# Optimization experiments

Measured on AMD Instinct MI355X. Metric: run time of the kernel, lower is better.

The kernel has to match this reference:

```python
import jax, jax.numpy as jnp
import numpy as np

N, C_IN, C_OUT = 8192, 256, 128
NEG_SLOPE = 0.2


def setup_inputs() -> dict:
    key = jax.random.key(0)
    k0, k1, k2, k3, k4 = jax.random.split(key, 5)
    x = jax.random.normal(k0, (N, C_IN), dtype=jnp.float32)
    # sparse-ish binary dense adjacency, avg degree ~32
    adj = (jax.random.uniform(k1, (N, N)) < (32.0 / N)).astype(jnp.float32)
    W = jax.random.normal(k2, (C_IN, C_OUT), dtype=jnp.float32) * 0.05
    att_src = jax.random.normal(k3, (C_OUT,), dtype=jnp.float32) * 0.1
    att_dst = jax.random.normal(k4, (C_OUT,), dtype=jnp.float32) * 0.1
    bias = jnp.zeros((C_OUT,), dtype=jnp.float32)
    return {"x": x, "adj": adj, "W": W, "att_src": att_src,
            "att_dst": att_dst, "bias": bias}


def reference(x, adj, W, att_src, att_dst, bias):
    n = adj.shape[0]
    idx = jnp.arange(n)
    adj = adj.at[idx, idx].set(1.0)          # add self loops
    h = x @ W                                 # [N, C_out]
    a_src = h @ att_src                       # [N]
    a_dst = h @ att_dst                       # [N]
    alpha = a_src[:, None] + a_dst[None, :]   # [N, N]
    alpha = jax.nn.leaky_relu(alpha, NEG_SLOPE)
    alpha = adj * jnp.exp(alpha)              # masked exp
    alpha = alpha / alpha.sum(axis=0, keepdims=True)  # column-normalize (dim=0)
    out = (adj * alpha).T @ h + bias          # [N, C_out]
    return out
```

## Files before the change

kernel.cpp:

```cpp
#include <hip/hip_runtime.h>
#include <hip/hip_bf16.h>

#define NN 8192
#define CIN 256
#define COUT 128
#define GR 32
#define GKT 64
#define CH 16
#define ICH (NN / CH)
#define KT 64
#define HTS 72

typedef unsigned short u16;
typedef _Float16 f16;
typedef __attribute__((ext_vector_type(8))) short short8;
typedef __attribute__((ext_vector_type(8))) _Float16 f16x8;
typedef __attribute__((ext_vector_type(16))) float f32x16;

__device__ __forceinline__ short8 pack8_bf16(const float* v) {
    union { __hip_bfloat162 b2[4]; short8 s; } u;
    #pragma unroll
    for (int q = 0; q < 4; ++q)
        u.b2[q] = __float22bfloat162_rn(make_float2(v[2 * q], v[2 * q + 1]));
    return u.s;
}

__global__ __launch_bounds__(256) void gemm_h(const float* __restrict__ x,
                                              const float* __restrict__ W,
                                              const float* __restrict__ att_src,
                                              const float* __restrict__ att_dst,
                                              u16* __restrict__ h_t,
                                              float* __restrict__ a_src,
                                              float* __restrict__ a_dst) {
    __shared__ float Wt[GKT * COUT];
    __shared__ float xt[GKT][GR + 4];
    __shared__ float ot[GR][COUT + 4];
    int tid = threadIdx.x;
    int i0 = blockIdx.x * GR;
    int tx = tid & 31, ty = tid >> 5;
    int c0 = tx * 4, r0 = ty * 4;
    int xr = tid >> 3, xk = (tid & 7) * 8;
    float acc[4][4] = {};

    for (int kt = 0; kt < CIN; kt += GKT) {
        float4 wv[8];
        #pragma unroll
        for (int j = 0; j < 8; ++j) {
            int f = j * 256 + tid;
            wv[j] = *(const float4*)&W[(size_t)(kt + (f >> 5)) * COUT + (f & 31) * 4];
        }
        float4 xv0 = *(const float4*)&x[(size_t)(i0 + xr) * CIN + kt + xk];
        float4 xv1 = *(const float4*)&x[(size_t)(i0 + xr) * CIN + kt + xk + 4];
        __syncthreads();
        #pragma unroll
        for (int j = 0; j < 8; ++j)
            *(float4*)&Wt[(j * 256 + tid) * 4] = wv[j];
        xt[xk + 0][xr] = xv0.x; xt[xk + 1][xr] = xv0.y;
        xt[xk + 2][xr] = xv0.z; xt[xk + 3][xr] = xv0.w;
        xt[xk + 4][xr] = xv1.x; xt[xk + 5][xr] = xv1.y;
        xt[xk + 6][xr] = xv1.z; xt[xk + 7][xr] = xv1.w;
        __syncthreads();
        #pragma unroll 8
        for (int k = 0; k < GKT; ++k) {
            float4 wk = *(const float4*)&Wt[k * COUT + c0];
            float4 xf = *(const float4*)&xt[k][r0];
            float xa[4] = {xf.x, xf.y, xf.z, xf.w};
            #pragma unroll
            for (int a = 0; a < 4; ++a) {
                acc[a][0] += xa[a] * wk.x; acc[a][1] += xa[a] * wk.y;
                acc[a][2] += xa[a] * wk.z; acc[a][3] += xa[a] * wk.w;
            }
        }
    }

    float4 asv = *(const float4*)&att_src[c0];
    float4 adv = *(const float4*)&att_dst[c0];
    #pragma unroll
    for (int a = 0; a < 4; ++a) {
        float4 o = make_float4(acc[a][0], acc[a][1], acc[a][2], acc[a][3]);
        *(float4*)&ot[r0 + a][c0] = o;
        float s = o.x * asv.x + o.y * asv.y + o.z * asv.z + o.w * asv.w;
        float d = o.x * adv.x + o.y * adv.y + o.z * adv.z + o.w * adv.w;
        #pragma unroll
        for (int m = 16; m >= 1; m >>= 1) {
            s += __shfl_xor(s, m, 32);
            d += __shfl_xor(d, m, 32);
        }
        if (tx == 0) {
            a_src[i0 + r0 + a] = s;
            a_dst[i0 + r0 + a] = d;
        }
    }
    __syncthreads();
    int c = tid >> 1, hf = tid & 1;
    float vals[16];
    #pragma unroll
    for (int q = 0; q < 16; ++q) vals[q] = ot[hf * 16 + q][c];
    *(short8*)(h_t + (size_t)c * NN + i0 + hf * 16)     = pack8_bf16(vals);
    *(short8*)(h_t + (size_t)c * NN + i0 + hf * 16 + 8) = pack8_bf16(vals + 8);
}

__global__ __launch_bounds__(256, 3) void gat_mm(const float* __restrict__ adj,
                                                 const u16* __restrict__ h_t,
                                                 const float* __restrict__ a_src,
                                                 const float* __restrict__ a_dst,
                                                 f16* __restrict__ pout,
                                                 float* __restrict__ pden) {
    __shared__ unsigned int maskS[KT * 4];
    __shared__ u16 htS[128 * HTS];
    __shared__ float asrcS[ICH];
    int tid = threadIdx.x;
    int lane = tid & 63, w = tid >> 6;
    int jb = blockIdx.x & 63, ch = blockIdx.x >> 6;
    int j0 = jb * 128;
    int i0 = ch * ICH;
    int half = lane >> 5;
    int jloc = w * 32 + (lane & 31);
    int gj = j0 + jloc;
    int slot = lane & 3;
    int kbit = jloc >> 2;
    float dj = a_dst[gj];
    if (tid < ICH / 4)
        ((float4*)asrcS)[tid] = ((const float4*)(a_src + i0))[tid];

    f32x16 acc[4];
    #pragma unroll
    for (int nt = 0; nt < 4; ++nt)
        #pragma unroll
        for (int q = 0; q < 16; ++q) acc[nt][q] = 0.f;
    float dsum = 0.f;
    __syncthreads();

    for (int s = 0; s < ICH / KT; ++s) {
        int ib = i0 + s * KT;
        float4 v[8];
        #pragma unroll
        for (int q = 0; q < 8; ++q) {
            int f = q * 256 + tid;
            v[q] = *(const float4*)&adj[(size_t)(ib + (f >> 5)) * NN + j0 + (f & 31) * 4];
        }
        short8 bv[4]; int bc[4], bi[4];
        #pragma unroll
        for (int q = 0; q < 4; ++q) {
            int p = q * 256 + tid;
            bc[q] = p >> 3; bi[q] = (p & 7) * 8;
            bv[q] = *(const short8*)(h_t + (size_t)bc[q] * NN + ib + bi[q]);
        }
        #pragma unroll
        for (int q = 0; q < 8; ++q) {
            unsigned long long b0 = __ballot(v[q].x != 0.f);
            unsigned long long b1 = __ballot(v[q].y != 0.f);
            unsigned long long b2 = __ballot(v[q].z != 0.f);
            unsigned long long b3 = __ballot(v[q].w != 0.f);
            unsigned long long bb = slot == 0 ? b0 : slot == 1 ? b1
                                  : slot == 2 ? b2 : b3;
            unsigned int mw = (unsigned int)(bb >> (half * 32));
            int R = q * 8 + w * 2 + half;
            if ((lane & 31) < 4) maskS[R * 4 + slot] = mw;
        }
        #pragma unroll
        for (int q = 0; q < 4; ++q)
            *(short8*)(htS + bc[q] * HTS + bi[q]) = bv[q];
        __syncthreads();

        #pragma unroll
        for (int kk = 0; kk < 4; ++kk) {
            int kb = kk * 16 + half * 8;
            int gib = ib + kb;
            short8 bf[4];
            #pragma unroll
            for (int nt = 0; nt < 4; ++nt)
                bf[nt] = *(const short8*)(htS + (nt * 32 + (lane & 31)) * HTS + kb);
            float pv[8];
            #pragma unroll
            for (int e = 0; e < 8; ++e) {
                unsigned int mw = maskS[(kb + e) * 4 + slot];
                float t = asrcS[s * KT + kb + e] + dj;
                float ev = __expf(fmaxf(t, 0.2f * t));
                bool on = ((mw >> kbit) & 1u) | (gib + e == gj);
                pv[e] = on ? ev : 0.f;
                dsum += pv[e];
            }
            short8 af = pack8_bf16(pv);
            #pragma unroll
            for (int nt = 0; nt < 4; ++nt)
                acc[nt] = __builtin_amdgcn_mfma_f32_32x32x16_bf16(af, bf[nt],
                                                                  acc[nt], 0, 0, 0);
        }
        __syncthreads();
    }

    #pragma unroll
    for (int nt = 0; nt < 4; ++nt) {
        int c = nt * 32 + (lane & 31);
        #pragma unroll
        for (int r = 0; r < 16; ++r) {
            int row = (r & 3) + 8 * (r >> 2) + 4 * half;
            int j = j0 + w * 32 + row;
            pout[((size_t)ch * NN + j) * COUT + c] = (f16)acc[nt][r];
        }
    }
    float dall = dsum + __shfl_xor(dsum, 32, 64);
    if (half == 0) pden[(size_t)ch * NN + gj] = dall;
}

__global__ __launch_bounds__(256) void gat_reduce(const f16* __restrict__ pout,
                                                  const float* __restrict__ pden,
                                                  const float* __restrict__ bias,
                                                  float* __restrict__ out) {
    int idx = blockIdx.x * 256 + threadIdx.x;
    int j = idx >> 4;
    int c8 = (idx & 15) * 8;
    float den = 0.f;
    #pragma unroll
    for (int ch = 0; ch < CH; ++ch) den += pden[(size_t)ch * NN + j];
    float s[8] = {};
    #pragma unroll
    for (int ch = 0; ch < CH; ++ch) {
        f16x8 pv = *(const f16x8*)(pout + ((size_t)ch * NN + j) * COUT + c8);
        #pragma unroll
        for (int q = 0; q < 8; ++q) s[q] += (float)pv[q];
    }
    float inv = 1.0f / den;
    float4 b0 = *(const float4*)&bias[c8];
    float4 b1 = *(const float4*)&bias[c8 + 4];
    float4 o0 = make_float4(s[0] * inv + b0.x, s[1] * inv + b0.y,
                            s[2] * inv + b0.z, s[3] * inv + b0.w);
    float4 o1 = make_float4(s[4] * inv + b1.x, s[5] * inv + b1.y,
                            s[6] * inv + b1.z, s[7] * inv + b1.w);
    *(float4*)&out[(size_t)j * COUT + c8]     = o0;
    *(float4*)&out[(size_t)j * COUT + c8 + 4] = o1;
}

extern "C" void kernel_launch(void* const* d_in, const int* in_sizes, int n_in,
                              void* d_out, int out_size, void* d_ws, size_t ws_size,
                              hipStream_t stream) {
    const float* x       = (const float*)d_in[0];
    const float* adj     = (const float*)d_in[1];
    const float* W       = (const float*)d_in[2];
    const float* att_src = (const float*)d_in[3];
    const float* att_dst = (const float*)d_in[4];
    const float* bias    = (const float*)d_in[5];
    float* out = (float*)d_out;

    u16*   h_t   = (u16*)d_ws;
    float* a_src = (float*)((char*)d_ws + (size_t)2 * 1024 * 1024);
    float* a_dst = a_src + NN;
    float* pden  = a_dst + NN;
    f16*   pout  = (f16*)(pden + (size_t)CH * NN);

    gemm_h    <<<NN / GR, 256, 0, stream>>>(x, W, att_src, att_dst, h_t, a_src, a_dst);
    gat_mm    <<<64 * CH, 256, 0, stream>>>(adj, h_t, a_src, a_dst, pout, pden);
    gat_reduce<<<NN * COUT / 8 / 256, 256, 0, stream>>>(pout, pden, bias, out);
}
```

Baseline: 407.0 us.

## Precompute adjacency bitmask in a separate pass and stream it into gat_mm

Adds an adj2mask kernel that reads the dense fp32 adjacency once, ballots nonzero entries into bit words, and writes them in a layout blocked by column tile (maskT). gat_mm then loads one 32-bit mask word per thread per k-step instead of eight float4 adjacency loads plus ballots. The main loop becomes lighter and less memory-bound. The cost is an extra kernel launch and a 8 MB mask write/read round trip; the full 256 MB adjacency is still read once, now with row-contiguous access.

Result: slower. 436.6 us (+7.3%).

```diff
diff --git a/kernel.cpp b/kernel.cpp
--- a/kernel.cpp
+++ b/kernel.cpp
@@ -23,6 +23,35 @@
     for (int q = 0; q < 4; ++q)
         u.b2[q] = __float22bfloat162_rn(make_float2(v[2 * q], v[2 * q + 1]));
     return u.s;
+}
+
+__global__ __launch_bounds__(256) void adj2mask(const float* __restrict__ adj,
+                                                unsigned int* __restrict__ maskT) {
+    int tid = threadIdx.x;
+    int lane = tid & 63, w = tid >> 6;
+    int i = blockIdx.x * 4 + w;
+    const float4* rowp = (const float4*)(adj + (size_t)i * NN);
+    int half = lane >> 5, slot = lane & 3;
+    bool writer = (lane & 31) < 4;
+    for (int it = 0; it < 32; it += 8) {
+        float4 v[8];
+        #pragma unroll
+        for (int q = 0; q < 8; ++q)
+            v[q] = rowp[(it + q) * 64 + lane];
+        #pragma unroll
+        for (int q = 0; q < 8; ++q) {
+            unsigned long long b0 = __ballot(v[q].x != 0.f);
+            unsigned long long b1 = __ballot(v[q].y != 0.f);
+            unsigned long long b2 = __ballot(v[q].z != 0.f);
+            unsigned long long b3 = __ballot(v[q].w != 0.f);
+            unsigned long long bb = slot == 0 ? b0 : slot == 1 ? b1
+                                  : slot == 2 ? b2 : b3;
+            unsigned int mw = (unsigned int)(bb >> (half * 32));
+            int jb = (it + q) * 2 + half;
+            if (writer)
+                maskT[((size_t)jb * NN + i) * 4 + slot] = mw;
+        }
+    }
 }
 
 __global__ __launch_bounds__(256) void gemm_h(const float* __restrict__ x,
@@ -100,7 +129,7 @@
     *(short8*)(h_t + (size_t)c * NN + i0 + hf * 16 + 8) = pack8_bf16(vals + 8);
 }
 
-__global__ __launch_bounds__(256, 3) void gat_mm(const float* __restrict__ adj,
+__global__ __launch_bounds__(256, 3) void gat_mm(const unsigned int* __restrict__ maskT,
                                                  const u16* __restrict__ h_t,
                                                  const float* __restrict__ a_src,
                                                  const float* __restrict__ a_dst,
@@ -133,12 +162,7 @@
 
     for (int s = 0; s < ICH / KT; ++s) {
         int ib = i0 + s * KT;
-        float4 v[8];
-        #pragma unroll
-        for (int q = 0; q < 8; ++q) {
-            int f = q * 256 + tid;
-            v[q] = *(const float4*)&adj[(size_t)(ib + (f >> 5)) * NN + j0 + (f & 31) * 4];
-        }
+        unsigned int mword = maskT[((size_t)jb * NN + ib) * 4 + tid];
         short8 bv[4]; int bc[4], bi[4];
         #pragma unroll
         for (int q = 0; q < 4; ++q) {
@@ -146,18 +170,7 @@
             bc[q] = p >> 3; bi[q] = (p & 7) * 8;
             bv[q] = *(const short8*)(h_t + (size_t)bc[q] * NN + ib + bi[q]);
         }
-        #pragma unroll
-        for (int q = 0; q < 8; ++q) {
-            unsigned long long b0 = __ballot(v[q].x != 0.f);
-            unsigned long long b1 = __ballot(v[q].y != 0.f);
-            unsigned long long b2 = __ballot(v[q].z != 0.f);
-            unsigned long long b3 = __ballot(v[q].w != 0.f);
-            unsigned long long bb = slot == 0 ? b0 : slot == 1 ? b1
-                                  : slot == 2 ? b2 : b3;
-            unsigned int mw = (unsigned int)(bb >> (half * 32));
-            int R = q * 8 + w * 2 + half;
-            if ((lane & 31) < 4) maskS[R * 4 + slot] = mw;
-        }
+        maskS[tid] = mword;
         #pragma unroll
         for (int q = 0; q < 4; ++q)
             *(short8*)(htS + bc[q] * HTS + bi[q]) = bv[q];
@@ -247,9 +260,11 @@
     float* a_src = (float*)((char*)d_ws + (size_t)2 * 1024 * 1024);
     float* a_dst = a_src + NN;
     float* pden  = a_dst + NN;
-    f16*   pout  = (f16*)(pden + (size_t)CH * NN);
-
+    unsigned int* maskT = (unsigned int*)(pden + (size_t)CH * NN);
+    f16*   pout  = (f16*)(maskT + (size_t)64 * NN * 4);
+
+    adj2mask  <<<NN / 4, 256, 0, stream>>>(adj, maskT);
     gemm_h    <<<NN / GR, 256, 0, stream>>>(x, W, att_src, att_dst, h_t, a_src, a_dst);
-    gat_mm    <<<64 * CH, 256, 0, stream>>>(adj, h_t, a_src, a_dst, pout, pden);
+    gat_mm    <<<64 * CH, 256, 0, stream>>>(maskT, h_t, a_src, a_dst, pout, pden);
     gat_reduce<<<NN * COUT / 8 / 256, 256, 0, stream>>>(pout, pden, bias, out);
 }
```
